# Kernel tuning notes

Measured on AMD Instinct MI355X. Metric: run time of the kernel, lower is better.

## Reference

```python
import jax, jax.numpy as jnp
import numpy as np

B, L, DIM, K = 2, 512, 128, 32
EPS = 1e-5  # torch LayerNorm default


def setup_inputs() -> dict:
    key = jax.random.key(0)
    ks = jax.random.split(key, 4)
    s = 1.0 / np.sqrt(DIM)
    s2 = 1.0 / np.sqrt(2 * DIM)
    return {
        "pair_repr": jax.random.normal(ks[0], (B, L, L, DIM), jnp.float32),
        "W_out": jax.random.uniform(ks[1], (DIM, DIM), jnp.float32, -s, s),
        "b_out": jnp.zeros((DIM,), jnp.float32),
        "W_in": jax.random.uniform(ks[2], (DIM, DIM), jnp.float32, -s, s),
        "b_in": jnp.zeros((DIM,), jnp.float32),
        "W_g": jax.random.uniform(ks[3], (2 * DIM, DIM), jnp.float32, -s2, s2),
        "b_g": jnp.zeros((DIM,), jnp.float32),
        "ln_w": jnp.ones((DIM,), jnp.float32),
        "ln_b": jnp.zeros((DIM,), jnp.float32),
    }


def reference(pair_repr, W_out, b_out, W_in, b_in, W_g, b_g, ln_w, ln_b):
    # Eval-mode deterministic sampling: torch.linspace(0, L-1, K).long()
    idx = jnp.floor(jnp.linspace(0.0, L - 1, K)).astype(jnp.int32)

    # Linear is affine, so mean(Linear(x)) == Linear(mean(x)); project after mean.
    out_mean = pair_repr[:, :, idx, :].mean(axis=2)          # (B, L, dim)
    out_agg = out_mean @ W_out + b_out                        # (B, L, dim)
    in_mean = pair_repr[:, idx, :, :].mean(axis=1)            # (B, L, dim)
    in_agg = in_mean @ W_in + b_in                            # (B, L, dim)

    # gate = sigmoid(Linear(cat(out_b, in_b))): split W_g to avoid materializing the 2*dim concat
    Wg_o, Wg_i = W_g[:DIM], W_g[DIM:]
    gate = jax.nn.sigmoid(
        (out_agg @ Wg_o)[:, :, None, :]
        + (in_agg @ Wg_i)[:, None, :, :]
        + b_g
    )                                                         # (B, L, L, dim)

    update = out_agg[:, :, None, :] + in_agg[:, None, :, :]   # (B, L, L, dim)
    x = pair_repr + gate * (update - pair_repr)

    # LayerNorm over last axis (biased variance, matching torch)
    mu = x.mean(axis=-1, keepdims=True)
    var = x.var(axis=-1, keepdims=True)
    return (x - mu) / jnp.sqrt(var + EPS) * ln_w + ln_b
```

## Files before the change

kernel.cpp:

```cpp
#include <hip/hip_runtime.h>

#define BB 2
#define LL 512
#define DIM 128
#define KK 32
#define EPSF 1e-5f

__global__ __launch_bounds__(DIM) void agg_gemm_kernel(
    const float* __restrict__ pair,
    const float* __restrict__ W_out, const float* __restrict__ b_out,
    const float* __restrict__ W_in,  const float* __restrict__ b_in,
    const float* __restrict__ W_g,
    float* __restrict__ agg,
    float* __restrict__ gpart)
{
    const int t    = threadIdx.x;
    const int bid  = blockIdx.x;
    const int path = bid >> 10;
    const int r    = bid & 1023;
    const int b    = r >> 9;
    const int q    = r & 511;

    __shared__ float sm[DIM];

    float acc = 0.f;
    if (path == 0) {
        const float* base = pair + ((long)(b * LL + q) * LL) * DIM + t;
#pragma unroll
        for (int k = 0; k < KK; ++k) {
            const int jj = (k * (LL - 1)) / (KK - 1);
            acc += base[(long)jj * DIM];
        }
    } else {
        const float* base = pair + (long)b * LL * LL * DIM + (long)q * DIM + t;
#pragma unroll
        for (int k = 0; k < KK; ++k) {
            const int jj = (k * (LL - 1)) / (KK - 1);
            acc += base[(long)jj * (LL * DIM)];
        }
    }
    sm[t] = acc * (1.0f / KK);
    __syncthreads();

    const float* W    = (path == 0) ? W_out : W_in;
    const float* bias = (path == 0) ? b_out : b_in;
    float a = bias[t];
#pragma unroll 8
    for (int k = 0; k < DIM; ++k)
        a += sm[k] * W[k * DIM + t];
    __syncthreads();
    sm[t] = a;
    agg[(long)path * BB * LL * DIM + (long)r * DIM + t] = a;
    __syncthreads();

    const float* Wg = W_g + path * DIM * DIM;
    float g = 0.f;
#pragma unroll 8
    for (int k = 0; k < DIM; ++k)
        g += sm[k] * Wg[k * DIM + t];
    gpart[(long)path * BB * LL * DIM + (long)r * DIM + t] = g;
}

__device__ __forceinline__ void load8c(const float* __restrict__ base,
                                       int e0, int e1, float* f) {
    const float4 a = *reinterpret_cast<const float4*>(base + e0);
    const float4 b = *reinterpret_cast<const float4*>(base + e1);
    f[0] = a.x; f[1] = a.y; f[2] = a.z; f[3] = a.w;
    f[4] = b.x; f[5] = b.y; f[6] = b.z; f[7] = b.w;
}

__global__ __launch_bounds__(256, 4) void fuse_ln_kernel(
    const float* __restrict__ pair,
    const float* __restrict__ out_agg, const float* __restrict__ in_agg,
    const float* __restrict__ go,      const float* __restrict__ gi,
    const float* __restrict__ b_g, const float* __restrict__ ln_w,
    const float* __restrict__ ln_b,
    float* __restrict__ out)
{
    const int tid    = threadIdx.x;
    const int lane16 = tid & 15;
    const int rloc   = tid >> 4;
    const int blk    = blockIdx.x;
    const int half   = blk & 1;
    const int bi     = blk >> 1;
    const int b      = bi >> 9;
    const int jbase  = half * (LL / 2);

    const int e0 = lane16 * 4;
    const int e1 = 64 + lane16 * 4;

    float gof[8], oaf[8], bg[8], lw[8], lb[8];
    load8c(go      + (long)bi * DIM, e0, e1, gof);
    load8c(out_agg + (long)bi * DIM, e0, e1, oaf);
    load8c(b_g,  e0, e1, bg);
    load8c(ln_w, e0, e1, lw);
    load8c(ln_b, e0, e1, lb);

    const long bL = (long)b * LL;

#pragma unroll 2
    for (int jt = 0; jt < (LL / 2) / 16; ++jt) {
        const int  j   = jbase + jt * 16 + rloc;
        const long row = (long)bi * LL + j;
        const long bj  = bL + j;

        float p[8], gif[8], iaf[8];
        load8c(pair   + row * DIM, e0, e1, p);
        load8c(gi     + bj  * DIM, e0, e1, gif);
        load8c(in_agg + bj  * DIM, e0, e1, iaf);

        float x[8];
        float sum = 0.f, ss = 0.f;
#pragma unroll
        for (int c = 0; c < 8; ++c) {
            const float z    = gof[c] + gif[c] + bg[c];
            const float e    = __builtin_amdgcn_exp2f(z * -1.442695041f);
            const float gate = __builtin_amdgcn_rcpf(1.0f + e);
            const float u    = oaf[c] + iaf[c];
            const float xv   = p[c] + gate * (u - p[c]);
            x[c] = xv;
            sum += xv;
            ss  += xv * xv;
        }

#pragma unroll
        for (int m = 1; m < 16; m <<= 1) {
            sum += __shfl_xor(sum, m);
            ss  += __shfl_xor(ss,  m);
        }
        const float mu   = sum * (1.0f / DIM);
        const float var  = ss * (1.0f / DIM) - mu * mu;
        const float rstd = rsqrtf(var + EPSF);

        float y[8];
#pragma unroll
        for (int c = 0; c < 8; ++c)
            y[c] = (x[c] - mu) * rstd * lw[c] + lb[c];

        float* op = out + row * DIM;
        *reinterpret_cast<float4*>(op + e0) = make_float4(y[0], y[1], y[2], y[3]);
        *reinterpret_cast<float4*>(op + e1) = make_float4(y[4], y[5], y[6], y[7]);
    }
}

extern "C" void kernel_launch(void* const* d_in, const int* in_sizes, int n_in,
                              void* d_out, int out_size, void* d_ws, size_t ws_size,
                              hipStream_t stream) {
    const float* pair  = (const float*)d_in[0];
    const float* W_out = (const float*)d_in[1];
    const float* b_out = (const float*)d_in[2];
    const float* W_in  = (const float*)d_in[3];
    const float* b_in  = (const float*)d_in[4];
    const float* W_g   = (const float*)d_in[5];
    const float* b_g   = (const float*)d_in[6];
    const float* ln_w  = (const float*)d_in[7];
    const float* ln_b  = (const float*)d_in[8];
    float* out = (float*)d_out;

    float* agg   = (float*)d_ws;
    float* gpart = agg + 2 * BB * LL * DIM;

    agg_gemm_kernel<<<2 * BB * LL, DIM, 0, stream>>>(
        pair, W_out, b_out, W_in, b_in, W_g, agg, gpart);

    fuse_ln_kernel<<<2 * BB * LL, 256, 0, stream>>>(
        pair,
        agg,   agg   + BB * LL * DIM,
        gpart, gpart + BB * LL * DIM,
        b_g, ln_w, ln_b, out);
}
```

Baseline: 484.7 us.

## Pack gate/agg rows together, use 32-lane rows and nontemporal pair/out traffic

The gate partial and the aggregate vectors for each row are interleaved into one 256-float packed record, so the fuse kernel reads one contiguous record per row. Each row is now handled by 32 lanes with one float4 each instead of 16 lanes with two, and the per-i gate constant is folded with b_g up front. Pair loads and output stores use nontemporal hints to avoid polluting the cache with streaming data. The occupancy hint on launch bounds is dropped, and the LayerNorm reduction needs one extra shuffle step.

```diff
diff --git a/kernel.cpp b/kernel.cpp
--- a/kernel.cpp
+++ b/kernel.cpp
@@ -6,13 +6,15 @@
 #define KK 32
 #define EPSF 1e-5f
 
+typedef float f32x4 __attribute__((ext_vector_type(4)));
+
 __global__ __launch_bounds__(DIM) void agg_gemm_kernel(
     const float* __restrict__ pair,
     const float* __restrict__ W_out, const float* __restrict__ b_out,
     const float* __restrict__ W_in,  const float* __restrict__ b_in,
     const float* __restrict__ W_g,
-    float* __restrict__ agg,
-    float* __restrict__ gpart)
+    float* __restrict__ bipack,
+    float* __restrict__ bjpack)
 {
     const int t    = threadIdx.x;
     const int bid  = blockIdx.x;
@@ -42,6 +44,8 @@
     sm[t] = acc * (1.0f / KK);
     __syncthreads();
 
+    float* pk = (path == 0 ? bipack : bjpack) + (long)r * 256;
+
     const float* W    = (path == 0) ? W_out : W_in;
     const float* bias = (path == 0) ? b_out : b_in;
     float a = bias[t];
@@ -50,7 +54,7 @@
         a += sm[k] * W[k * DIM + t];
     __syncthreads();
     sm[t] = a;
-    agg[(long)path * BB * LL * DIM + (long)r * DIM + t] = a;
+    pk[128 + t] = a;
     __syncthreads();
 
     const float* Wg = W_g + path * DIM * DIM;
@@ -58,73 +62,62 @@
 #pragma unroll 8
     for (int k = 0; k < DIM; ++k)
         g += sm[k] * Wg[k * DIM + t];
-    gpart[(long)path * BB * LL * DIM + (long)r * DIM + t] = g;
+    pk[t] = g;
 }
 
-__device__ __forceinline__ void load8c(const float* __restrict__ base,
-                                       int e0, int e1, float* f) {
-    const float4 a = *reinterpret_cast<const float4*>(base + e0);
-    const float4 b = *reinterpret_cast<const float4*>(base + e1);
-    f[0] = a.x; f[1] = a.y; f[2] = a.z; f[3] = a.w;
-    f[4] = b.x; f[5] = b.y; f[6] = b.z; f[7] = b.w;
-}
-
-__global__ __launch_bounds__(256, 4) void fuse_ln_kernel(
+__global__ __launch_bounds__(256) void fuse_ln_kernel(
     const float* __restrict__ pair,
-    const float* __restrict__ out_agg, const float* __restrict__ in_agg,
-    const float* __restrict__ go,      const float* __restrict__ gi,
+    const float* __restrict__ bipack, const float* __restrict__ bjpack,
     const float* __restrict__ b_g, const float* __restrict__ ln_w,
     const float* __restrict__ ln_b,
     float* __restrict__ out)
 {
-    const int tid    = threadIdx.x;
-    const int lane16 = tid & 15;
-    const int rloc   = tid >> 4;
-    const int blk    = blockIdx.x;
-    const int half   = blk & 1;
-    const int bi     = blk >> 1;
-    const int b      = bi >> 9;
-    const int jbase  = half * (LL / 2);
+    const int tid  = threadIdx.x;
+    const int l32  = tid & 31;
+    const int rloc = tid >> 5;
+    const int blk  = blockIdx.x;
+    const int half = blk & 1;
+    const int bi   = blk >> 1;
+    const int b    = bi >> 9;
+    const int jbase = half * (LL / 2);
+    const int e    = l32 * 4;
 
-    const int e0 = lane16 * 4;
-    const int e1 = 64 + lane16 * 4;
-
-    float gof[8], oaf[8], bg[8], lw[8], lb[8];
-    load8c(go      + (long)bi * DIM, e0, e1, gof);
-    load8c(out_agg + (long)bi * DIM, e0, e1, oaf);
-    load8c(b_g,  e0, e1, bg);
-    load8c(ln_w, e0, e1, lw);
-    load8c(ln_b, e0, e1, lb);
+    const f32x4 go4 = *reinterpret_cast<const f32x4*>(bipack + (long)bi * 256 + e);
+    const f32x4 oa4 = *reinterpret_cast<const f32x4*>(bipack + (long)bi * 256 + 128 + e);
+    const f32x4 bg4 = *reinterpret_cast<const f32x4*>(b_g  + e);
+    const f32x4 lw4 = *reinterpret_cast<const f32x4*>(ln_w + e);
+    const f32x4 lb4 = *reinterpret_cast<const f32x4*>(ln_b + e);
+    const f32x4 zc4 = go4 + bg4;
 
     const long bL = (long)b * LL;
 
 #pragma unroll 2
-    for (int jt = 0; jt < (LL / 2) / 16; ++jt) {
-        const int  j   = jbase + jt * 16 + rloc;
+    for (int it = 0; it < (LL / 2) / 8; ++it) {
+        const int  j   = jbase + it * 8 + rloc;
         const long row = (long)bi * LL + j;
         const long bj  = bL + j;
 
-        float p[8], gif[8], iaf[8];
-        load8c(pair   + row * DIM, e0, e1, p);
-        load8c(gi     + bj  * DIM, e0, e1, gif);
-        load8c(in_agg + bj  * DIM, e0, e1, iaf);
+        const f32x4 pv = __builtin_nontemporal_load(
+            reinterpret_cast<const f32x4*>(pair + row * DIM + e));
+        const f32x4 gv = *reinterpret_cast<const f32x4*>(bjpack + bj * 256 + e);
+        const f32x4 iv = *reinterpret_cast<const f32x4*>(bjpack + bj * 256 + 128 + e);
 
-        float x[8];
+        f32x4 x;
         float sum = 0.f, ss = 0.f;
 #pragma unroll
-        for (int c = 0; c < 8; ++c) {
-            const float z    = gof[c] + gif[c] + bg[c];
-            const float e    = __builtin_amdgcn_exp2f(z * -1.442695041f);
-            const float gate = __builtin_amdgcn_rcpf(1.0f + e);
-            const float u    = oaf[c] + iaf[c];
-            const float xv   = p[c] + gate * (u - p[c]);
+        for (int c = 0; c < 4; ++c) {
+            const float z    = zc4[c] + gv[c];
+            const float ex   = __builtin_amdgcn_exp2f(z * -1.442695041f);
+            const float gate = __builtin_amdgcn_rcpf(1.0f + ex);
+            const float u    = oa4[c] + iv[c];
+            const float xv   = pv[c] + gate * (u - pv[c]);
             x[c] = xv;
             sum += xv;
             ss  += xv * xv;
         }
 
 #pragma unroll
-        for (int m = 1; m < 16; m <<= 1) {
+        for (int m = 1; m < 32; m <<= 1) {
             sum += __shfl_xor(sum, m);
             ss  += __shfl_xor(ss,  m);
         }
@@ -132,14 +125,13 @@
         const float var  = ss * (1.0f / DIM) - mu * mu;
         const float rstd = rsqrtf(var + EPSF);
 
-        float y[8];
+        f32x4 y;
 #pragma unroll
-        for (int c = 0; c < 8; ++c)
-            y[c] = (x[c] - mu) * rstd * lw[c] + lb[c];
+        for (int c = 0; c < 4; ++c)
+            y[c] = (x[c] - mu) * rstd * lw4[c] + lb4[c];
 
-        float* op = out + row * DIM;
-        *reinterpret_cast<float4*>(op + e0) = make_float4(y[0], y[1], y[2], y[3]);
-        *reinterpret_cast<float4*>(op + e1) = make_float4(y[4], y[5], y[6], y[7]);
+        __builtin_nontemporal_store(
+            y, reinterpret_cast<f32x4*>(out + row * DIM + e));
     }
 }
 
@@ -157,15 +149,12 @@
     const float* ln_b  = (const float*)d_in[8];
     float* out = (float*)d_out;
 
-    float* agg   = (float*)d_ws;
-    float* gpart = agg + 2 * BB * LL * DIM;
+    float* bipack = (float*)d_ws;
+    float* bjpack = bipack + BB * LL * 256;
 
     agg_gemm_kernel<<<2 * BB * LL, DIM, 0, stream>>>(
-        pair, W_out, b_out, W_in, b_in, W_g, agg, gpart);
+        pair, W_out, b_out, W_in, b_in, W_g, bipack, bjpack);
 
     fuse_ln_kernel<<<2 * BB * LL, 256, 0, stream>>>(
-        pair,
-        agg,   agg   + BB * LL * DIM,
-        gpart, gpart + BB * LL * DIM,
-        b_g, ln_w, ln_b, out);
+        pair, bipack, bjpack, b_g, ln_w, ln_b, out);
 }
```

Measured after the change: 481.0 us. About the same (-0.8%).
